# Kernel tuning notes

Hardware: AMD Instinct MI355X
Metric: run time of the kernel (lower is better)

Reference implementation:

```python
import jax, jax.numpy as jnp
import numpy as np

B = 16384  # batch
H = 1024   # n_hidden == dim_att


def setup_inputs() -> dict:
    key = jax.random.key(0)
    ks = jax.random.split(key, 9)
    x = jax.random.normal(ks[0], (B, H), jnp.float32)
    alpha = jax.random.normal(ks[1], (B, H), jnp.float32)
    aa = jax.random.normal(ks[2], (B, H), jnp.float32) * 0.1
    # bb accumulates sums of positive exponentials -> keep it positive
    bb = jax.random.uniform(ks[3], (B, H), jnp.float32) + 0.5
    pp = jax.random.normal(ks[4], (B, H), jnp.float32)
    # parameters, initialized exactly as in the torch module
    ratio_0_to_1 = 0.5
    ratio_1_to_almost0 = 0.5
    ddd = jnp.arange(H, dtype=jnp.float32) / H
    _x = jnp.arange(H, dtype=jnp.float32) / (H - 1)
    time_decay = -5.0 + 8.0 * _x ** (0.7 + 1.3 * ratio_0_to_1)
    zigzag = ((jnp.arange(H) + 1) % 3 - 1).astype(jnp.float32) * 0.5
    time_first = jnp.full((H,), np.float32(np.log(0.3))) + zigzag
    time_mix_k = ddd ** ratio_1_to_almost0
    time_mix_v = ddd ** ratio_1_to_almost0 + 0.3 * ratio_0_to_1
    time_mix_r = ddd ** (0.5 * ratio_1_to_almost0)
    s = 1.0 / np.sqrt(H)
    Wk = jax.random.normal(ks[5], (H, H), jnp.float32) * s
    Wv = jax.random.normal(ks[6], (H, H), jnp.float32) * s
    Wr = jax.random.normal(ks[7], (H, H), jnp.float32) * s
    Wo = jax.random.normal(ks[8], (H, H), jnp.float32) * s
    return {"x": x, "alpha": alpha, "aa": aa, "bb": bb, "pp": pp,
            "time_decay": time_decay, "time_first": time_first,
            "time_mix_k": time_mix_k, "time_mix_v": time_mix_v,
            "time_mix_r": time_mix_r,
            "Wk": Wk, "Wv": Wv, "Wr": Wr, "Wo": Wo}


def reference(x, alpha, aa, bb, pp, time_decay, time_first,
              time_mix_k, time_mix_v, time_mix_r, Wk, Wv, Wr, Wo):
    # token-shift style mixing with previous input (alpha)
    xk = x * time_mix_k + alpha * (1.0 - time_mix_k)
    xv = x * time_mix_v + alpha * (1.0 - time_mix_v)
    xr = x * time_mix_r + alpha * (1.0 - time_mix_r)
    # nn.Linear(y = x @ W.T), all [B,H] @ [H,H]
    r = jax.nn.sigmoid(xr @ Wr.T)
    k = xk @ Wk.T
    v = xv @ Wv.T
    # WKV output with log-sum-exp stabilization
    ww = time_first + k
    qq = jnp.maximum(pp, ww)
    e1 = jnp.exp(pp - qq)
    e2 = jnp.exp(ww - qq)
    wkv = (e1 * aa + e2 * v) / (e1 * bb + e2)
    # state update with decay
    ww2 = pp + time_decay
    qq2 = jnp.maximum(ww2, k)
    e1b = jnp.exp(ww2 - qq2)
    e2b = jnp.exp(k - qq2)
    next_aa = e1b * aa + e2b * v
    next_bb = e1b * bb + e2b
    out = (r * wkv) @ Wo.T
    return (out, x, next_aa, next_bb, qq2)
```

## Files before the change

kernel.cpp:

```cpp
#include <hip/hip_runtime.h>
#include <stdint.h>

#define BDIM 16384
#define HDIM 1024
#define BHSZ (BDIM * HDIM)

typedef unsigned short u16;
typedef __attribute__((ext_vector_type(8))) short short8;
typedef __attribute__((ext_vector_type(4))) float floatx4;

typedef __attribute__((address_space(1))) const void gvoid;
typedef __attribute__((address_space(3))) void lvoid;

__device__ __forceinline__ float bf2f(u16 u) {
  union { uint32_t i; float f; } c; c.i = ((uint32_t)u) << 16; return c.f;
}
__device__ __forceinline__ u16 f2bf(float f) {
  union { float f; uint32_t i; } c; c.f = f;
  uint32_t r = (c.i + 0x7fffu + ((c.i >> 16) & 1u)) >> 16;
  return (u16)r;
}
__device__ __forceinline__ uint4 pack8(const float* f) {
  uint4 v;
  v.x = (uint32_t)f2bf(f[0]) | ((uint32_t)f2bf(f[1]) << 16);
  v.y = (uint32_t)f2bf(f[2]) | ((uint32_t)f2bf(f[3]) << 16);
  v.z = (uint32_t)f2bf(f[4]) | ((uint32_t)f2bf(f[5]) << 16);
  v.w = (uint32_t)f2bf(f[6]) | ((uint32_t)f2bf(f[7]) << 16);
  return v;
}

__global__ __launch_bounds__(256) void f2b_kernel(
    const float* __restrict__ in, u16* __restrict__ out) {
  const int idx = (blockIdx.x * 256 + threadIdx.x) * 8;
  float4 v0 = *(const float4*)(in + idx);
  float4 v1 = *(const float4*)(in + idx + 4);
  float f[8] = {v0.x, v0.y, v0.z, v0.w, v1.x, v1.y, v1.z, v1.w};
  *(uint4*)(out + idx) = pack8(f);
}

__global__ __launch_bounds__(256) void mix_kernel(
    const float* __restrict__ x, const float* __restrict__ alpha,
    const float* __restrict__ tm, u16* __restrict__ xmix,
    float* __restrict__ xcopy) {
  const int idx = (blockIdx.x * 256 + threadIdx.x) * 8;
  const int h = idx & (HDIM - 1);
  float4 x0 = *(const float4*)(x + idx);
  float4 x1 = *(const float4*)(x + idx + 4);
  float4 a0 = *(const float4*)(alpha + idx);
  float4 a1 = *(const float4*)(alpha + idx + 4);
  float4 t0 = *(const float4*)(tm + h);
  float4 t1 = *(const float4*)(tm + h + 4);
  float xf[8] = {x0.x, x0.y, x0.z, x0.w, x1.x, x1.y, x1.z, x1.w};
  float af[8] = {a0.x, a0.y, a0.z, a0.w, a1.x, a1.y, a1.z, a1.w};
  float tf[8] = {t0.x, t0.y, t0.z, t0.w, t1.x, t1.y, t1.z, t1.w};
  float of[8];
#pragma unroll
  for (int j = 0; j < 8; ++j) of[j] = xf[j] * tf[j] + af[j] * (1.0f - tf[j]);
  *(uint4*)(xmix + idx) = pack8(of);
  if (xcopy) {
    *(float4*)(xcopy + idx) = x0;
    *(float4*)(xcopy + idx + 4) = x1;
  }
}

__device__ __forceinline__ void gemm_core(
    const u16* __restrict__ A, const u16* __restrict__ W, int K,
    int mBase, int nBase, u16* As, u16* Bs, floatx4 acc[4][4]) {
  const int tid = threadIdx.x;
  const int lane = tid & 63;
  const int wave = tid >> 6;
  const int wm = (wave >> 1) * 64;
  const int wn = (wave & 1) * 64;
  const int lm = lane & 15;
  const int lk = (lane >> 4) * 8;

#pragma unroll
  for (int i = 0; i < 4; ++i)
#pragma unroll
    for (int j = 0; j < 4; ++j) acc[i][j] = (floatx4){0.f, 0.f, 0.f, 0.f};

  for (int k0 = 0; k0 < K; k0 += 32) {
#pragma unroll
    for (int p = 0; p < 2; ++p) {
      const int g = tid + p * 256;
      const int row = g >> 2;
      const int col = (g & 3) * 8;
      const u16* ga = A + (size_t)(mBase + row) * K + (k0 + col);
      const u16* gb = W + (size_t)(nBase + row) * K + (k0 + col);
      __builtin_amdgcn_global_load_lds((gvoid*)ga, (lvoid*)(As + g * 8), 16, 0, 0);
      __builtin_amdgcn_global_load_lds((gvoid*)gb, (lvoid*)(Bs + g * 8), 16, 0, 0);
    }
    __syncthreads();

    short8 a[4], b[4];
#pragma unroll
    for (int i = 0; i < 4; ++i)
      a[i] = *(const short8*)(As + (wm + i * 16 + lm) * 32 + lk);
#pragma unroll
    for (int i = 0; i < 4; ++i)
      b[i] = *(const short8*)(Bs + (wn + i * 16 + lm) * 32 + lk);
#pragma unroll
    for (int mi = 0; mi < 4; ++mi)
#pragma unroll
      for (int ni = 0; ni < 4; ++ni)
        acc[mi][ni] = __builtin_amdgcn_mfma_f32_16x16x32_bf16(
            a[mi], b[ni], acc[mi][ni], 0, 0, 0);
    __syncthreads();
  }
}


__global__ __launch_bounds__(256) void gemm_bf16out(
    const u16* __restrict__ A, const u16* __restrict__ W,
    u16* __restrict__ C, int K, int N) {
  __shared__ u16 As[128 * 32];
  __shared__ u16 Bs[128 * 32];
  floatx4 acc[4][4];
  const int mBase = blockIdx.y * 128;
  const int nBase = blockIdx.x * 128;
  gemm_core(A, W, K, mBase, nBase, As, Bs, acc);
  const int lane = threadIdx.x & 63;
  const int wave = threadIdx.x >> 6;
  const int wm = (wave >> 1) * 64, wn = (wave & 1) * 64;
  const int lm = lane & 15, rBase = (lane >> 4) * 4;
#pragma unroll
  for (int mi = 0; mi < 4; ++mi)
#pragma unroll
    for (int ni = 0; ni < 4; ++ni) {
      const int gn = nBase + wn + ni * 16 + lm;
#pragma unroll
      for (int r = 0; r < 4; ++r) {
        const int gm = mBase + wm + mi * 16 + rBase + r;
        C[(size_t)gm * N + gn] = f2bf(acc[mi][ni][r]);
      }
    }
}

__global__ __launch_bounds__(256) void gemm_f32out(
    const u16* __restrict__ A, const u16* __restrict__ W,
    float* __restrict__ C, int K, int N) {
  __shared__ u16 As[128 * 32];
  __shared__ u16 Bs[128 * 32];
  floatx4 acc[4][4];
  const int mBase = blockIdx.y * 128;
  const int nBase = blockIdx.x * 128;
  gemm_core(A, W, K, mBase, nBase, As, Bs, acc);
  const int lane = threadIdx.x & 63;
  const int wave = threadIdx.x >> 6;
  const int wm = (wave >> 1) * 64, wn = (wave & 1) * 64;
  const int lm = lane & 15, rBase = (lane >> 4) * 4;
#pragma unroll
  for (int mi = 0; mi < 4; ++mi)
#pragma unroll
    for (int ni = 0; ni < 4; ++ni) {
      const int gn = nBase + wn + ni * 16 + lm;
#pragma unroll
      for (int r = 0; r < 4; ++r) {
        const int gm = mBase + wm + mi * 16 + rBase + r;
        C[(size_t)gm * N + gn] = acc[mi][ni][r];
      }
    }
}

__global__ __launch_bounds__(256) void gemm_r_wkv(
    const u16* __restrict__ A, const u16* __restrict__ W,
    u16* __restrict__ kbuf, const u16* __restrict__ vbuf,
    const float* __restrict__ aa, const float* __restrict__ bb,
    const float* __restrict__ pp, const float* __restrict__ tdec,
    const float* __restrict__ tfirst, float* __restrict__ naa,
    float* __restrict__ nbb, float* __restrict__ qq2, int K, int N) {
  __shared__ u16 As[128 * 32];
  __shared__ u16 Bs[128 * 32];
  floatx4 acc[4][4];
  const int mBase = blockIdx.y * 128;
  const int nBase = blockIdx.x * 128;
  gemm_core(A, W, K, mBase, nBase, As, Bs, acc);
  const int lane = threadIdx.x & 63;
  const int wave = threadIdx.x >> 6;
  const int wm = (wave >> 1) * 64, wn = (wave & 1) * 64;
  const int lm = lane & 15, rBase = (lane >> 4) * 4;
#pragma unroll
  for (int mi = 0; mi < 4; ++mi)
#pragma unroll
    for (int ni = 0; ni < 4; ++ni) {
      const int gn = nBase + wn + ni * 16 + lm;
      const float td = tdec[gn];
      const float tf = tfirst[gn];
#pragma unroll
      for (int r = 0; r < 4; ++r) {
        const int gm = mBase + wm + mi * 16 + rBase + r;
        const size_t off = (size_t)gm * N + gn;
        const float kk = bf2f(kbuf[off]);
        const float vv = bf2f(vbuf[off]);
        const float A_ = aa[off];
        const float B_ = bb[off];
        const float P_ = pp[off];
        const float rr = 1.0f / (1.0f + __expf(-acc[mi][ni][r]));
        const float ww = tf + kk;
        const float qq = fmaxf(P_, ww);
        const float e1 = __expf(P_ - qq);
        const float e2 = __expf(ww - qq);
        const float wkv = (e1 * A_ + e2 * vv) / (e1 * B_ + e2);
        kbuf[off] = f2bf(rr * wkv);
        const float ww2 = P_ + td;
        const float q = fmaxf(ww2, kk);
        const float e1b = __expf(ww2 - q);
        const float e2b = __expf(kk - q);
        naa[off] = e1b * A_ + e2b * vv;
        nbb[off] = e1b * B_ + e2b;
        qq2[off] = q;
      }
    }
}

extern "C" void kernel_launch(void* const* d_in, const int* in_sizes, int n_in,
                              void* d_out, int out_size, void* d_ws, size_t ws_size,
                              hipStream_t stream) {
  const float* x      = (const float*)d_in[0];
  const float* alpha  = (const float*)d_in[1];
  const float* aa     = (const float*)d_in[2];
  const float* bb     = (const float*)d_in[3];
  const float* pp     = (const float*)d_in[4];
  const float* tdec   = (const float*)d_in[5];
  const float* tfirst = (const float*)d_in[6];
  const float* tmk    = (const float*)d_in[7];
  const float* tmv    = (const float*)d_in[8];
  const float* tmr    = (const float*)d_in[9];
  const float* Wk     = (const float*)d_in[10];
  const float* Wv     = (const float*)d_in[11];
  const float* Wr     = (const float*)d_in[12];
  const float* Wo     = (const float*)d_in[13];

  float* out  = (float*)d_out;
  float* outx = out + (size_t)BHSZ;
  float* naa  = out + 2 * (size_t)BHSZ;
  float* nbb  = out + 3 * (size_t)BHSZ;
  float* qq2  = out + 4 * (size_t)BHSZ;

  u16* mixbuf = (u16*)d_ws;
  u16* kbuf   = mixbuf + (size_t)BHSZ;
  u16* vbuf   = mixbuf + 2 * (size_t)BHSZ;
  u16* wbuf   = mixbuf + 3 * (size_t)BHSZ;

  const dim3 gEW(BHSZ / (256 * 8));
  const dim3 gW(HDIM * HDIM / (256 * 8));
  const dim3 gG(HDIM / 128, BDIM / 128);

  mix_kernel<<<gEW, 256, 0, stream>>>(x, alpha, tmk, mixbuf, outx);
  f2b_kernel<<<gW, 256, 0, stream>>>(Wk, wbuf);
  gemm_bf16out<<<gG, 256, 0, stream>>>(mixbuf, wbuf, kbuf, HDIM, HDIM);
  mix_kernel<<<gEW, 256, 0, stream>>>(x, alpha, tmv, mixbuf, nullptr);
  f2b_kernel<<<gW, 256, 0, stream>>>(Wv, wbuf);
  gemm_bf16out<<<gG, 256, 0, stream>>>(mixbuf, wbuf, vbuf, HDIM, HDIM);
  mix_kernel<<<gEW, 256, 0, stream>>>(x, alpha, tmr, mixbuf, nullptr);
  f2b_kernel<<<gW, 256, 0, stream>>>(Wr, wbuf);
  gemm_r_wkv<<<gG, 256, 0, stream>>>(mixbuf, wbuf, kbuf, vbuf, aa, bb, pp,
                                     tdec, tfirst, naa, nbb, qq2, HDIM, HDIM);
  f2b_kernel<<<gW, 256, 0, stream>>>(Wo, wbuf);
  gemm_f32out<<<gG, 256, 0, stream>>>(kbuf, wbuf, out, HDIM, HDIM);
}
```

Before: 982.2 us.

## Fuse token-mix passes and split WKV epilogue into coalesced elementwise kernel

The three mix kernels become one pass that reads x and alpha once and writes all three bf16 mixed inputs. The r GEMM now only applies the sigmoid and stores bf16 r. A separate vectorized kernel then computes WKV and the state update with coalesced 8-wide loads, replacing the strided scalar epilogue loads. Output buffers are reused as scratch for intermediates, which adds one extra bf16 round trip for r and one more launch.

```diff
diff --git a/kernel.cpp b/kernel.cpp
--- a/kernel.cpp
+++ b/kernel.cpp
@@ -28,39 +28,58 @@
   v.w = (uint32_t)f2bf(f[6]) | ((uint32_t)f2bf(f[7]) << 16);
   return v;
 }
+__device__ __forceinline__ void unpack8(uint4 v, float* f) {
+  const uint32_t w[4] = {v.x, v.y, v.z, v.w};
+#pragma unroll
+  for (int j = 0; j < 4; ++j) {
+    f[2 * j]     = bf2f((u16)(w[j] & 0xffffu));
+    f[2 * j + 1] = bf2f((u16)(w[j] >> 16));
+  }
+}
+__device__ __forceinline__ void ld8(const float* p, float* f) {
+  float4 v0 = *(const float4*)(p);
+  float4 v1 = *(const float4*)(p + 4);
+  f[0] = v0.x; f[1] = v0.y; f[2] = v0.z; f[3] = v0.w;
+  f[4] = v1.x; f[5] = v1.y; f[6] = v1.z; f[7] = v1.w;
+}
+__device__ __forceinline__ void st8(float* p, const float* f) {
+  *(float4*)(p)     = (float4){f[0], f[1], f[2], f[3]};
+  *(float4*)(p + 4) = (float4){f[4], f[5], f[6], f[7]};
+}
 
 __global__ __launch_bounds__(256) void f2b_kernel(
     const float* __restrict__ in, u16* __restrict__ out) {
   const int idx = (blockIdx.x * 256 + threadIdx.x) * 8;
-  float4 v0 = *(const float4*)(in + idx);
-  float4 v1 = *(const float4*)(in + idx + 4);
-  float f[8] = {v0.x, v0.y, v0.z, v0.w, v1.x, v1.y, v1.z, v1.w};
+  float f[8];
+  ld8(in + idx, f);
   *(uint4*)(out + idx) = pack8(f);
 }
 
-__global__ __launch_bounds__(256) void mix_kernel(
+__global__ __launch_bounds__(256) void mix_all_kernel(
     const float* __restrict__ x, const float* __restrict__ alpha,
-    const float* __restrict__ tm, u16* __restrict__ xmix,
+    const float* __restrict__ tmk, const float* __restrict__ tmv,
+    const float* __restrict__ tmr, u16* __restrict__ xk,
+    u16* __restrict__ xv, u16* __restrict__ xr,
     float* __restrict__ xcopy) {
   const int idx = (blockIdx.x * 256 + threadIdx.x) * 8;
   const int h = idx & (HDIM - 1);
-  float4 x0 = *(const float4*)(x + idx);
-  float4 x1 = *(const float4*)(x + idx + 4);
-  float4 a0 = *(const float4*)(alpha + idx);
-  float4 a1 = *(const float4*)(alpha + idx + 4);
-  float4 t0 = *(const float4*)(tm + h);
-  float4 t1 = *(const float4*)(tm + h + 4);
-  float xf[8] = {x0.x, x0.y, x0.z, x0.w, x1.x, x1.y, x1.z, x1.w};
-  float af[8] = {a0.x, a0.y, a0.z, a0.w, a1.x, a1.y, a1.z, a1.w};
-  float tf[8] = {t0.x, t0.y, t0.z, t0.w, t1.x, t1.y, t1.z, t1.w};
-  float of[8];
-#pragma unroll
-  for (int j = 0; j < 8; ++j) of[j] = xf[j] * tf[j] + af[j] * (1.0f - tf[j]);
-  *(uint4*)(xmix + idx) = pack8(of);
-  if (xcopy) {
-    *(float4*)(xcopy + idx) = x0;
-    *(float4*)(xcopy + idx + 4) = x1;
+  float xf[8], af[8], tk[8], tv[8], tr[8];
+  ld8(x + idx, xf);
+  ld8(alpha + idx, af);
+  ld8(tmk + h, tk);
+  ld8(tmv + h, tv);
+  ld8(tmr + h, tr);
+  float ok[8], ov[8], orr[8];
+#pragma unroll
+  for (int j = 0; j < 8; ++j) {
+    ok[j]  = xf[j] * tk[j] + af[j] * (1.0f - tk[j]);
+    ov[j]  = xf[j] * tv[j] + af[j] * (1.0f - tv[j]);
+    orr[j] = xf[j] * tr[j] + af[j] * (1.0f - tr[j]);
   }
+  *(uint4*)(xk + idx) = pack8(ok);
+  *(uint4*)(xv + idx) = pack8(ov);
+  *(uint4*)(xr + idx) = pack8(orr);
+  st8(xcopy + idx, xf);
 }
 
 __device__ __forceinline__ void gemm_core(
@@ -136,6 +155,33 @@
     }
 }
 
+__global__ __launch_bounds__(256) void gemm_sig_bf16out(
+    const u16* __restrict__ A, const u16* __restrict__ W,
+    u16* __restrict__ C, int K, int N) {
+  __shared__ u16 As[128 * 32];
+  __shared__ u16 Bs[128 * 32];
+  floatx4 acc[4][4];
+  const int mBase = blockIdx.y * 128;
+  const int nBase = blockIdx.x * 128;
+  gemm_core(A, W, K, mBase, nBase, As, Bs, acc);
+  const int lane = threadIdx.x & 63;
+  const int wave = threadIdx.x >> 6;
+  const int wm = (wave >> 1) * 64, wn = (wave & 1) * 64;
+  const int lm = lane & 15, rBase = (lane >> 4) * 4;
+#pragma unroll
+  for (int mi = 0; mi < 4; ++mi)
+#pragma unroll
+    for (int ni = 0; ni < 4; ++ni) {
+      const int gn = nBase + wn + ni * 16 + lm;
+#pragma unroll
+      for (int r = 0; r < 4; ++r) {
+        const int gm = mBase + wm + mi * 16 + rBase + r;
+        const float rr = 1.0f / (1.0f + __expf(-acc[mi][ni][r]));
+        C[(size_t)gm * N + gn] = f2bf(rr);
+      }
+    }
+}
+
 __global__ __launch_bounds__(256) void gemm_f32out(
     const u16* __restrict__ A, const u16* __restrict__ W,
     float* __restrict__ C, int K, int N) {
@@ -162,55 +208,47 @@
     }
 }
 
-__global__ __launch_bounds__(256) void gemm_r_wkv(
-    const u16* __restrict__ A, const u16* __restrict__ W,
-    u16* __restrict__ kbuf, const u16* __restrict__ vbuf,
-    const float* __restrict__ aa, const float* __restrict__ bb,
-    const float* __restrict__ pp, const float* __restrict__ tdec,
-    const float* __restrict__ tfirst, float* __restrict__ naa,
-    float* __restrict__ nbb, float* __restrict__ qq2, int K, int N) {
-  __shared__ u16 As[128 * 32];
-  __shared__ u16 Bs[128 * 32];
-  floatx4 acc[4][4];
-  const int mBase = blockIdx.y * 128;
-  const int nBase = blockIdx.x * 128;
-  gemm_core(A, W, K, mBase, nBase, As, Bs, acc);
-  const int lane = threadIdx.x & 63;
-  const int wave = threadIdx.x >> 6;
-  const int wm = (wave >> 1) * 64, wn = (wave & 1) * 64;
-  const int lm = lane & 15, rBase = (lane >> 4) * 4;
-#pragma unroll
-  for (int mi = 0; mi < 4; ++mi)
-#pragma unroll
-    for (int ni = 0; ni < 4; ++ni) {
-      const int gn = nBase + wn + ni * 16 + lm;
-      const float td = tdec[gn];
-      const float tf = tfirst[gn];
-#pragma unroll
-      for (int r = 0; r < 4; ++r) {
-        const int gm = mBase + wm + mi * 16 + rBase + r;
-        const size_t off = (size_t)gm * N + gn;
-        const float kk = bf2f(kbuf[off]);
-        const float vv = bf2f(vbuf[off]);
-        const float A_ = aa[off];
-        const float B_ = bb[off];
-        const float P_ = pp[off];
-        const float rr = 1.0f / (1.0f + __expf(-acc[mi][ni][r]));
-        const float ww = tf + kk;
-        const float qq = fmaxf(P_, ww);
-        const float e1 = __expf(P_ - qq);
-        const float e2 = __expf(ww - qq);
-        const float wkv = (e1 * A_ + e2 * vv) / (e1 * B_ + e2);
-        kbuf[off] = f2bf(rr * wkv);
-        const float ww2 = P_ + td;
-        const float q = fmaxf(ww2, kk);
-        const float e1b = __expf(ww2 - q);
-        const float e2b = __expf(kk - q);
-        naa[off] = e1b * A_ + e2b * vv;
-        nbb[off] = e1b * B_ + e2b;
-        qq2[off] = q;
-      }
-    }
+__global__ __launch_bounds__(256) void wkv_kernel(
+    const u16* __restrict__ rb, u16* __restrict__ kb,
+    const u16* __restrict__ vb, const float* __restrict__ aa,
+    const float* __restrict__ bb, const float* __restrict__ pp,
+    const float* __restrict__ tdec, const float* __restrict__ tfirst,
+    float* __restrict__ naa, float* __restrict__ nbb,
+    float* __restrict__ qq2) {
+  const int idx = (blockIdx.x * 256 + threadIdx.x) * 8;
+  const int h = idx & (HDIM - 1);
+  float rf[8], kf[8], vf[8], af[8], bfv[8], pf[8], tdf[8], tff[8];
+  unpack8(*(const uint4*)(rb + idx), rf);
+  unpack8(*(const uint4*)(kb + idx), kf);
+  unpack8(*(const uint4*)(vb + idx), vf);
+  ld8(aa + idx, af);
+  ld8(bb + idx, bfv);
+  ld8(pp + idx, pf);
+  ld8(tdec + h, tdf);
+  ld8(tfirst + h, tff);
+  float rw[8], na[8], nb[8], q2[8];
+#pragma unroll
+  for (int j = 0; j < 8; ++j) {
+    const float kk = kf[j], vv = vf[j];
+    const float A_ = af[j], B_ = bfv[j], P_ = pf[j];
+    const float ww = tff[j] + kk;
+    const float qq = fmaxf(P_, ww);
+    const float e1 = __expf(P_ - qq);
+    const float e2 = __expf(ww - qq);
+    const float wkvv = (e1 * A_ + e2 * vv) / (e1 * B_ + e2);
+    rw[j] = rf[j] * wkvv;
+    const float ww2 = P_ + tdf[j];
+    const float q = fmaxf(ww2, kk);
+    const float e1b = __expf(ww2 - q);
+    const float e2b = __expf(kk - q);
+    na[j] = e1b * A_ + e2b * vv;
+    nb[j] = e1b * B_ + e2b;
+    q2[j] = q;
+  }
+  *(uint4*)(kb + idx) = pack8(rw);
+  st8(naa + idx, na);
+  st8(nbb + idx, nb);
+  st8(qq2 + idx, q2);
 }
 
 extern "C" void kernel_launch(void* const* d_in, const int* in_sizes, int n_in,
@@ -237,25 +275,29 @@
   float* nbb  = out + 3 * (size_t)BHSZ;
   float* qq2  = out + 4 * (size_t)BHSZ;
 
-  u16* mixbuf = (u16*)d_ws;
-  u16* kbuf   = mixbuf + (size_t)BHSZ;
-  u16* vbuf   = mixbuf + 2 * (size_t)BHSZ;
-  u16* wbuf   = mixbuf + 3 * (size_t)BHSZ;
+  u16* xrb = (u16*)d_ws;
+  u16* kb  = xrb + (size_t)BHSZ;
+  u16* vb  = kb + (size_t)BHSZ;
+  u16* wb  = vb + (size_t)BHSZ;
+
+  u16* xkb = (u16*)naa;
+  u16* xvb = (u16*)qq2;
+  u16* rb  = (u16*)out;
 
   const dim3 gEW(BHSZ / (256 * 8));
   const dim3 gW(HDIM * HDIM / (256 * 8));
   const dim3 gG(HDIM / 128, BDIM / 128);
 
-  mix_kernel<<<gEW, 256, 0, stream>>>(x, alpha, tmk, mixbuf, outx);
-  f2b_kernel<<<gW, 256, 0, stream>>>(Wk, wbuf);
-  gemm_bf16out<<<gG, 256, 0, stream>>>(mixbuf, wbuf, kbuf, HDIM, HDIM);
-  mix_kernel<<<gEW, 256, 0, stream>>>(x, alpha, tmv, mixbuf, nullptr);
-  f2b_kernel<<<gW, 256, 0, stream>>>(Wv, wbuf);
-  gemm_bf16out<<<gG, 256, 0, stream>>>(mixbuf, wbuf, vbuf, HDIM, HDIM);
-  mix_kernel<<<gEW, 256, 0, stream>>>(x, alpha, tmr, mixbuf, nullptr);
-  f2b_kernel<<<gW, 256, 0, stream>>>(Wr, wbuf);
-  gemm_r_wkv<<<gG, 256, 0, stream>>>(mixbuf, wbuf, kbuf, vbuf, aa, bb, pp,
-                                     tdec, tfirst, naa, nbb, qq2, HDIM, HDIM);
-  f2b_kernel<<<gW, 256, 0, stream>>>(Wo, wbuf);
-  gemm_f32out<<<gG, 256, 0, stream>>>(kbuf, wbuf, out, HDIM, HDIM);
-}
+  mix_all_kernel<<<gEW, 256, 0, stream>>>(x, alpha, tmk, tmv, tmr,
+                                          xkb, xvb, xrb, outx);
+  f2b_kernel<<<gW, 256, 0, stream>>>(Wk, wb);
+  gemm_bf16out<<<gG, 256, 0, stream>>>(xkb, wb, kb, HDIM, HDIM);
+  f2b_kernel<<<gW, 256, 0, stream>>>(Wv, wb);
+  gemm_bf16out<<<gG, 256, 0, stream>>>(xvb, wb, vb, HDIM, HDIM);
+  f2b_kernel<<<gW, 256, 0, stream>>>(Wr, wb);
+  gemm_sig_bf16out<<<gG, 256, 0, stream>>>(xrb, wb, rb, HDIM, HDIM);
+  wkv_kernel<<<gEW, 256, 0, stream>>>(rb, kb, vb, aa, bb, pp, tdec, tfirst,
+                                      naa, nbb, qq2);
+  f2b_kernel<<<gW, 256, 0, stream>>>(Wo, wb);
+  gemm_f32out<<<gG, 256, 0, stream>>>(kb, wb, out, HDIM, HDIM);
+}
```

Measured after the change: 882.1 us. -10.2%, faster.
